# Kernel tuning notes

Hardware: AMD Instinct MI355X
Metric: run time of the kernel (lower is better)

The kernel has to match this reference:

```python
import jax, jax.numpy as jnp
import numpy as np

NUM_NEIGHBORS = 9  # cfg['num_neighbors']


def _cdist(a, b):
    """Euclidean cdist. a: [..., M, D], b: [..., N, D] -> [..., M, N]."""
    a2 = jnp.sum(a * a, axis=-1)[..., :, None]
    b2 = jnp.sum(b * b, axis=-1)[..., None, :]
    ab = jnp.einsum('...md,...nd->...mn', a, b)
    return jnp.sqrt(jnp.maximum(a2 + b2 - 2.0 * ab, 0.0))


def setup_inputs() -> dict:
    key = jax.random.key(0)
    k1, k2 = jax.random.split(key)
    B, P, D, N = 8, 784, 384, 16384
    embedding = jax.random.normal(k1, (B * P, D), dtype=jnp.float32)
    embedding_coreset = jax.random.normal(k2, (N, D), dtype=jnp.float32)
    return {"embedding": embedding, "embedding_coreset": embedding_coreset, "batch_size": B}


def reference(embedding, embedding_coreset, batch_size):
    D = embedding.shape[-1]
    # 1-NN of every patch against the coreset
    dists = _cdist(embedding, embedding_coreset)          # [B*P, N]
    patch_scores = jnp.min(dists, axis=1).reshape(batch_size, -1)   # [B, P]
    locations = jnp.argmin(dists, axis=1).reshape(batch_size, -1)   # [B, P]

    b = jnp.arange(batch_size)
    max_patches = jnp.argmax(patch_scores, axis=1)        # [B]
    emb = embedding.reshape(batch_size, -1, D)            # [B, P, D]
    max_feats = emb[b, max_patches]                       # [B, D]
    score = patch_scores[b, max_patches]                  # [B]
    nn_index = locations[b, max_patches]                  # [B]
    nn_sample = embedding_coreset[nn_index]               # [B, D]

    # k-NN of the nearest coreset sample within the coreset (support set)
    d_nn = _cdist(nn_sample, embedding_coreset)           # [B, N]
    _, support = jax.lax.top_k(-d_nn, NUM_NEIGHBORS)      # smallest dists, ascending -> [B, K]
    support_feats = embedding_coreset[support]            # [B, K, D]

    # distances from max patch feature to the support samples
    d_sup = _cdist(max_feats[:, None, :], support_feats)[:, 0, :]  # [B, K]
    weights = (1.0 - jax.nn.softmax(d_sup, axis=1))[:, 0]          # [B]
    return weights * score
```

## Files before the change

kernel.cpp:

```cpp
#include <hip/hip_runtime.h>
#include <hip/hip_bf16.h>
#include <math.h>

#define M_TOTAL 6272
#define N_CS    16384
#define D_DIM   384
#define BATCH   8
#define P_PATCH 784
#define KNN     9

#define MTILES  (M_TOTAL / 128)
#define NTILES2 (N_CS / 128)
#define NBLK    (M_TOTAL / 4)
#define PBB     196

typedef _Float16 half8 __attribute__((ext_vector_type(8)));
typedef float    floatx4 __attribute__((ext_vector_type(4)));

__device__ __forceinline__ void async_copy16(const void* g, void* l) {
    __builtin_amdgcn_global_load_lds(
        (const __attribute__((address_space(1))) void*)g,
        (__attribute__((address_space(3))) void*)l, 16, 0, 0);
}

__device__ __forceinline__ unsigned long long shfl_xor_u64(unsigned long long v, int mk) {
    int lo = __shfl_xor((int)(unsigned)v, mk, 64);
    int hi = __shfl_xor((int)(unsigned)(v >> 32), mk, 64);
    return ((unsigned long long)(unsigned)hi << 32) | (unsigned)lo;
}

__global__ void convert_all_kernel(const float* __restrict__ emb,
                                   const float* __restrict__ cs,
                                   _Float16* __restrict__ embh,
                                   _Float16* __restrict__ csh,
                                   float* __restrict__ cnorm) {
    int w = threadIdx.x >> 6, lane = threadIdx.x & 63;
    int row = blockIdx.x * 4 + w;
    if (row >= N_CS + M_TOTAL) return;
    bool is_cs = row < N_CS;
    const float* r = (is_cs ? cs + (size_t)row * D_DIM
                            : emb + (size_t)(row - N_CS) * D_DIM) + lane * 6;
    float2 a = *(const float2*)r;
    float2 b = *(const float2*)(r + 2);
    float2 c = *(const float2*)(r + 4);
    union { _Float16 h[2]; unsigned u; } p0, p1, p2;
    p0.h[0] = (_Float16)a.x; p0.h[1] = (_Float16)a.y;
    p1.h[0] = (_Float16)b.x; p1.h[1] = (_Float16)b.y;
    p2.h[0] = (_Float16)c.x; p2.h[1] = (_Float16)c.y;
    unsigned* dst = (unsigned*)(is_cs ? csh + (size_t)row * D_DIM
                                      : embh + (size_t)(row - N_CS) * D_DIM) + lane * 3;
    dst[0] = p0.u; dst[1] = p1.u; dst[2] = p2.u;
    if (is_cs) {
        float s = a.x * a.x + a.y * a.y + b.x * b.x + b.y * b.y + c.x * c.x + c.y * c.y;
#pragma unroll
        for (int mk = 1; mk <= 32; mk <<= 1) s += __shfl_xor(s, mk, 64);
        if (lane == 0) cnorm[row] = s;
    }
}

__global__ __launch_bounds__(256, 3) void mindist_mfma_kernel(
    const _Float16* __restrict__ embh, const _Float16* __restrict__ csh,
    const float* __restrict__ cnorm,
    float* __restrict__ pvals, int* __restrict__ pidx) {
    __shared__ _Float16 As[128 * 64];
    __shared__ _Float16 Bs[128 * 64];
    __shared__ float smv[128 * 2];
    __shared__ int   smi[128 * 2];

    const int b    = blockIdx.x;
    const int bx   = b >> 7;
    const int by   = ((b & 7) << 4) | ((b >> 3) & 15);
    const int tid  = threadIdx.x;
    const int lane = tid & 63;
    const int w    = tid >> 6;
    const int wr   = w >> 1, wc = w & 1;
    const int prow0 = bx * 128;
    const int nbase = by * 128;
    const int q   = lane >> 4;
    const int cl  = lane & 15;

    floatx4 acc[4][4];
#pragma unroll
    for (int mi = 0; mi < 4; ++mi)
#pragma unroll
        for (int nj = 0; nj < 4; ++nj) acc[mi][nj] = (floatx4){0.f, 0.f, 0.f, 0.f};

    const int srow = lane >> 3;
    const int scol = ((lane & 7) ^ srow) * 8;

#define STAGE(KK)                                                             \
    {                                                                         \
        _Pragma("unroll")                                                     \
        for (int i = 0; i < 8; ++i) {                                         \
            int t = (w & 1) * 8 + i;                 \
            int r = t * 8 + srow;                                             \
            if (w < 2) {                                                      \
                async_copy16(csh + (size_t)(nbase + r) * D_DIM + (KK) + scol, \
                             &As[t * 512 + lane * 8]);                        \
            } else {                                                          \
                async_copy16(embh + (size_t)(prow0 + r) * D_DIM + (KK) + scol,\
                             &Bs[t * 512 + lane * 8]);                        \
            }                                                                 \
        }                                                                     \
    }

#define COMPUTE()                                                             \
    {                                                                         \
        _Pragma("unroll")                                                     \
        for (int ks = 0; ks < 2; ++ks) {                                      \
            half8 af[4], bf[4];                                               \
            _Pragma("unroll")                                                 \
            for (int mi = 0; mi < 4; ++mi) {                                  \
                int R = wr * 64 + mi * 16 + cl;                               \
                int p = (ks * 4 + q) ^ (R & 7);                               \
                af[mi] = *(const half8*)&As[R * 64 + p * 8];                  \
            }                                                                 \
            _Pragma("unroll")                                                 \
            for (int nj = 0; nj < 4; ++nj) {                                  \
                int C = wc * 64 + nj * 16 + cl;                               \
                int p = (ks * 4 + q) ^ (C & 7);                               \
                bf[nj] = *(const half8*)&Bs[C * 64 + p * 8];                  \
            }                                                                 \
            _Pragma("unroll")                                                 \
            for (int mi = 0; mi < 4; ++mi)                                    \
                _Pragma("unroll")                                             \
                for (int nj = 0; nj < 4; ++nj)                                \
                    acc[mi][nj] = __builtin_amdgcn_mfma_f32_16x16x32_f16(     \
                        af[mi], bf[nj], acc[mi][nj], 0, 0, 0);                \
        }                                                                     \
    }

#pragma unroll 1
    for (int kk = 0; kk < D_DIM; kk += 64) {
        __syncthreads();
        STAGE(kk);
        __syncthreads();
        COMPUTE();
    }
#undef STAGE
#undef COMPUTE

    float cn16[4][4];
#pragma unroll
    for (int mi = 0; mi < 4; ++mi)
#pragma unroll
        for (int r = 0; r < 4; ++r)
            cn16[mi][r] = cnorm[nbase + wr * 64 + mi * 16 + q * 4 + r];

    const int nb_lane = nbase + wr * 64 + q * 4;
#pragma unroll
    for (int nj = 0; nj < 4; ++nj) {
        float v = 3.4e38f; int idx = 0x7fffffff;
#pragma unroll
        for (int mi = 0; mi < 4; ++mi)
#pragma unroll
            for (int r = 0; r < 4; ++r) {
                float d = cn16[mi][r] - 2.f * acc[mi][nj][r];
                if (d < v) { v = d; idx = nb_lane + mi * 16 + r; }
            }
#pragma unroll
        for (int mk = 16; mk <= 32; mk <<= 1) {
            float v2 = __shfl_xor(v, mk, 64);
            int   i2 = __shfl_xor(idx, mk, 64);
            if (v2 < v || (v2 == v && i2 < idx)) { v = v2; idx = i2; }
        }
        if (q == 0) {
            int pl = wc * 64 + nj * 16 + cl;
            smv[pl * 2 + wr] = v;
            smi[pl * 2 + wr] = idx;
        }
    }
    __syncthreads();
    if (tid < 128) {
        float v = smv[tid * 2];      int i = smi[tid * 2];
        float v1 = smv[tid * 2 + 1]; int i1 = smi[tid * 2 + 1];
        if (v1 < v) { v = v1; i = i1; }
        pvals[(size_t)(prow0 + tid) * NTILES2 + by] = v;
        pidx[(size_t)(prow0 + tid) * NTILES2 + by]  = i;
    }
}

__global__ void reduce_rescore_kernel(const float* __restrict__ pvals,
                                      const int* __restrict__ pidx,
                                      const float* __restrict__ emb,
                                      const float* __restrict__ cs,
                                      int* __restrict__ loc,
                                      unsigned long long* __restrict__ partial) {
    __shared__ unsigned long long keys[4];
    int w = threadIdx.x >> 6, lane = threadIdx.x & 63;
    int m = blockIdx.x * 4 + w;
    float v = pvals[(size_t)m * NTILES2 + lane];
    int   i = pidx[(size_t)m * NTILES2 + lane];
    {
        float v1 = pvals[(size_t)m * NTILES2 + lane + 64];
        int   i1 = pidx[(size_t)m * NTILES2 + lane + 64];
        if (v1 < v) { v = v1; i = i1; }
    }
#pragma unroll
    for (int mk = 1; mk <= 32; mk <<= 1) {
        float v2 = __shfl_xor(v, mk, 64);
        int   i2 = __shfl_xor(i, mk, 64);
        if (v2 < v || (v2 == v && i2 < i)) { v = v2; i = i2; }
    }
    const float* a = emb + (size_t)m * D_DIM;
    const float* bp = cs + (size_t)i * D_DIM;
    float s = 0.f;
#pragma unroll
    for (int t = 0; t < D_DIM / 64; ++t) {
        float d = a[lane + t * 64] - bp[lane + t * 64];
        s += d * d;
    }
#pragma unroll
    for (int mk = 1; mk <= 32; mk <<= 1) s += __shfl_xor(s, mk, 64);
    if (lane == 0) {
        float sc = sqrtf(s);
        loc[m] = i;
        int p = m % P_PATCH;
        keys[w] = ((unsigned long long)__float_as_uint(sc) << 32) |
                  (unsigned)(0x7fffffff - p);
    }
    __syncthreads();
    if (threadIdx.x == 0) {
        unsigned long long k = keys[0];
        if (keys[1] > k) k = keys[1];
        if (keys[2] > k) k = keys[2];
        if (keys[3] > k) k = keys[3];
        partial[blockIdx.x] = k;
    }
}

__global__ void dnn_kernel(const float* __restrict__ cs,
                           const float* __restrict__ cnorm,
                           const unsigned long long* __restrict__ partial,
                           const int* __restrict__ loc,
                           float* __restrict__ dmat) {
    __shared__ int bnnS[BATCH];
    {
        int bb = threadIdx.x >> 5, l32 = threadIdx.x & 31;
        unsigned long long best = 0ull;
        for (int j = l32; j < PBB; j += 32) {
            unsigned long long k = partial[bb * PBB + j];
            if (k > best) best = k;
        }
#pragma unroll
        for (int mk = 1; mk <= 16; mk <<= 1) {
            unsigned long long o = shfl_xor_u64(best, mk);
            if (o > best) best = o;
        }
        if (l32 == 0) {
            int p = 0x7fffffff - (unsigned)(best & 0xffffffffull);
            bnnS[bb] = loc[bb * P_PATCH + p];
        }
    }
    __syncthreads();

    int lane = threadIdx.x & 63;
    int gw = (blockIdx.x * 256 + threadIdx.x) >> 6;
    float qv[BATCH][6];
#pragma unroll
    for (int b = 0; b < BATCH; ++b) {
        const float* qr = cs + (size_t)bnnS[b] * D_DIM + lane * 6;
#pragma unroll
        for (int j = 0; j < 6; ++j) qv[b][j] = qr[j];
    }
    for (int n = gw; n < N_CS; n += 1024) {
        const float* r = cs + (size_t)n * D_DIM + lane * 6;
        float x[6];
#pragma unroll
        for (int j = 0; j < 6; ++j) x[j] = r[j];
        float s[BATCH];
#pragma unroll
        for (int b = 0; b < BATCH; ++b) {
            float t = 0.f;
#pragma unroll
            for (int j = 0; j < 6; ++j) t += x[j] * qv[b][j];
            s[b] = t;
        }
#pragma unroll
        for (int b = 0; b < BATCH; ++b)
#pragma unroll
            for (int mk = 1; mk <= 32; mk <<= 1) s[b] += __shfl_xor(s[b], mk, 64);
        if (lane < BATCH) {
            float sv = s[0];
#pragma unroll
            for (int b = 1; b < BATCH; ++b) sv = (lane == b) ? s[b] : sv;
            dmat[(size_t)lane * N_CS + n] = cnorm[n] - 2.f * sv;
        }
    }
}

__device__ inline void merge9(float* av, int* ai, const float* bv, const int* bi) {
    float mv[KNN]; int mi[KNN];
    int x = 0, y = 0;
#pragma unroll
    for (int k = 0; k < KNN; ++k) {
        bool ta = (av[x] < bv[y]) || (av[x] == bv[y] && ai[x] < bi[y]);
        if (ta) { mv[k] = av[x]; mi[k] = ai[x]; ++x; }
        else    { mv[k] = bv[y]; mi[k] = bi[y]; ++y; }
    }
#pragma unroll
    for (int k = 0; k < KNN; ++k) { av[k] = mv[k]; ai[k] = mi[k]; }
}

__global__ void top9_final_kernel(const float* __restrict__ dmat,
                                  const float* __restrict__ emb,
                                  const float* __restrict__ cs,
                                  const unsigned long long* __restrict__ partial,
                                  float* __restrict__ out) {
    int b = blockIdx.x;
    int tid = threadIdx.x;
    __shared__ float lv[512][KNN];
    __shared__ int   li[512][KNN];
    __shared__ float mf[D_DIM];
    __shared__ float dsup[KNN];
    __shared__ float bscoreS;
    __shared__ int   bpatchS;

    if (tid < 64) {
        unsigned long long best = 0ull;
        for (int j = tid; j < PBB; j += 64) {
            unsigned long long k = partial[b * PBB + j];
            if (k > best) best = k;
        }
#pragma unroll
        for (int mk = 1; mk <= 32; mk <<= 1) {
            unsigned long long o = shfl_xor_u64(best, mk);
            if (o > best) best = o;
        }
        if (tid == 0) {
            bpatchS = 0x7fffffff - (unsigned)(best & 0xffffffffull);
            bscoreS = __uint_as_float((unsigned)(best >> 32));
        }
    }
    __syncthreads();
    int mp = bpatchS;
    const float* frow = emb + (size_t)(b * P_PATCH + mp) * D_DIM;
    for (int i = tid; i < D_DIM; i += 512) mf[i] = frow[i];

    float tv[KNN]; int ti[KNN];
#pragma unroll
    for (int k = 0; k < KNN; ++k) { tv[k] = 3.4e38f; ti[k] = 0x7fffffff; }
    for (int n = tid; n < N_CS; n += 512) {
        float d = dmat[(size_t)b * N_CS + n];
        if (d < tv[KNN - 1] || (d == tv[KNN - 1] && n < ti[KNN - 1])) {
            tv[KNN - 1] = d; ti[KNN - 1] = n;
#pragma unroll
            for (int k = KNN - 1; k > 0; --k) {
                if (tv[k] < tv[k - 1] || (tv[k] == tv[k - 1] && ti[k] < ti[k - 1])) {
                    float fv = tv[k]; tv[k] = tv[k - 1]; tv[k - 1] = fv;
                    int   iv = ti[k]; ti[k] = ti[k - 1]; ti[k - 1] = iv;
                }
            }
        }
    }
#pragma unroll
    for (int k = 0; k < KNN; ++k) { lv[tid][k] = tv[k]; li[tid][k] = ti[k]; }
    __syncthreads();
    for (int off = 256; off > 0; off >>= 1) {
        if (tid < off) {
            float av[KNN]; int ai[KNN]; float bv2[KNN]; int bi2[KNN];
#pragma unroll
            for (int k = 0; k < KNN; ++k) {
                av[k]  = lv[tid][k];        ai[k]  = li[tid][k];
                bv2[k] = lv[tid + off][k];  bi2[k] = li[tid + off][k];
            }
            merge9(av, ai, bv2, bi2);
#pragma unroll
            for (int k = 0; k < KNN; ++k) { lv[tid][k] = av[k]; li[tid][k] = ai[k]; }
        }
        __syncthreads();
    }
    {
        int k      = tid >> 5;
        int lane32 = tid & 31;
        if (k < KNN) {
            int idx = li[0][k];
            const float* r = cs + (size_t)idx * D_DIM;
            float s = 0.f;
            for (int i = lane32; i < D_DIM; i += 32) {
                float df = mf[i] - r[i];
                s += df * df;
            }
#pragma unroll
            for (int mk = 1; mk <= 16; mk <<= 1) s += __shfl_xor(s, mk, 64);
            if (lane32 == 0) dsup[k] = sqrtf(fmaxf(s, 0.f));
        }
    }
    __syncthreads();
    if (tid == 0) {
        float mx = dsup[0];
        for (int k = 1; k < KNN; ++k) mx = fmaxf(mx, dsup[k]);
        float sum = 0.f, e0 = 0.f;
        for (int k = 0; k < KNN; ++k) {
            float e = expf(dsup[k] - mx);
            sum += e;
            if (k == 0) e0 = e;
        }
        out[b] = (1.f - e0 / sum) * bscoreS;
    }
}

extern "C" void kernel_launch(void* const* d_in, const int* in_sizes, int n_in,
                              void* d_out, int out_size, void* d_ws, size_t ws_size,
                              hipStream_t stream) {
    (void)in_sizes; (void)n_in; (void)out_size; (void)ws_size;
    const float* emb = (const float*)d_in[0];
    const float* cs  = (const float*)d_in[1];
    float* out = (float*)d_out;

    char* p = (char*)d_ws;
    float* cnorm  = (float*)p;  p += (size_t)N_CS * 4;
    float* pvals  = (float*)p;  p += (size_t)M_TOTAL * NTILES2 * 4;
    int*   pidx   = (int*)p;    p += (size_t)M_TOTAL * NTILES2 * 4;
    int*   loc    = (int*)p;    p += (size_t)M_TOTAL * 4;
    p = (char*)(((size_t)p + 7) & ~(size_t)7);
    unsigned long long* partial = (unsigned long long*)p; p += NBLK * 8;
    float* dmat   = (float*)p;  p += (size_t)BATCH * N_CS * 4;
    p = (char*)(((size_t)p + 15) & ~(size_t)15);
    _Float16* embh = (_Float16*)p; p += (size_t)M_TOTAL * D_DIM * 2;
    _Float16* csh  = (_Float16*)p; p += (size_t)N_CS * D_DIM * 2;

    {
        int rows = N_CS + M_TOTAL;
        convert_all_kernel<<<(rows + 3) / 4, 256, 0, stream>>>(emb, cs, embh, csh, cnorm);
    }
    mindist_mfma_kernel<<<MTILES * NTILES2, 256, 0, stream>>>(embh, csh, cnorm,
                                                              pvals, pidx);
    reduce_rescore_kernel<<<NBLK, 256, 0, stream>>>(pvals, pidx, emb, cs, loc, partial);
    dnn_kernel<<<256, 256, 0, stream>>>(cs, cnorm, partial, loc, dmat);
    top9_final_kernel<<<BATCH, 512, 0, stream>>>(dmat, emb, cs, partial, out);
}
```

Baseline: 252.0 us.

## Double-buffer LDS with 256x128 tiles and interleave async loads with MFMA phases

The min-distance GEMM now uses 512-thread blocks over 256 coreset by 128 patch tiles, so each block holds twice as many coreset columns and makes half as many partial results. LDS is double-buffered, and the async global-to-LDS copies for the next K tile are spread across four MFMA phases with explicit barriers, setprio and sched_barrier. This hides load latency behind compute and improves reuse of the patch tile. In exchange it uses more LDS per block and lowers occupancy, and it relies on hand-placed waitcnt and barrier ordering, which is fragile.

```diff
diff --git a/kernel.cpp b/kernel.cpp
--- a/kernel.cpp
+++ b/kernel.cpp
@@ -10,7 +10,7 @@
 #define KNN     9
 
 #define MTILES  (M_TOTAL / 128)
-#define NTILES2 (N_CS / 128)
+#define NTILES2 (N_CS / 256)
 #define NBLK    (M_TOTAL / 4)
 #define PBB     196
 
@@ -58,26 +58,30 @@
     }
 }
 
-__global__ __launch_bounds__(256, 3) void mindist_mfma_kernel(
+__global__ __launch_bounds__(512, 2) void mindist_mfma_kernel(
     const _Float16* __restrict__ embh, const _Float16* __restrict__ csh,
     const float* __restrict__ cnorm,
     float* __restrict__ pvals, int* __restrict__ pidx) {
-    __shared__ _Float16 As[128 * 64];
-    __shared__ _Float16 Bs[128 * 64];
-    __shared__ float smv[128 * 2];
-    __shared__ int   smi[128 * 2];
+    __shared__ _Float16 As0[256 * 64];
+    __shared__ _Float16 As1[256 * 64];
+    __shared__ _Float16 Bs0[128 * 64];
+    __shared__ _Float16 Bs1[128 * 64];
+    __shared__ float smv[128 * 4];
+    __shared__ int   smi[128 * 4];
 
     const int b    = blockIdx.x;
-    const int bx   = b >> 7;
-    const int by   = ((b & 7) << 4) | ((b >> 3) & 15);
+    const int bx   = b >> 6;
+    const int by   = ((b & 7) << 3) | ((b >> 3) & 7);
     const int tid  = threadIdx.x;
     const int lane = tid & 63;
     const int w    = tid >> 6;
-    const int wr   = w >> 1, wc = w & 1;
+    const int wr   = w >> 1;
+    const int wc   = w & 1;
     const int prow0 = bx * 128;
-    const int nbase = by * 128;
+    const int nbase = by * 256;
     const int q   = lane >> 4;
     const int cl  = lane & 15;
+    const int xsw = cl & 7;
 
     floatx4 acc[4][4];
 #pragma unroll
@@ -88,57 +92,84 @@
     const int srow = lane >> 3;
     const int scol = ((lane & 7) ^ srow) * 8;
 
-#define STAGE(KK)                                                             \
+#define STAGE_A(AS, KK, i)                                                    \
+    async_copy16(csh + (size_t)(nbase + (w * 4 + (i)) * 8 + srow) * D_DIM     \
+                     + (KK) + scol,                                           \
+                 &AS[(w * 4 + (i)) * 512 + lane * 8])
+#define STAGE_B(BS, KK, i)                                                    \
+    async_copy16(embh + (size_t)(prow0 + (w * 2 + (i)) * 8 + srow) * D_DIM    \
+                      + (KK) + scol,                                          \
+                 &BS[(w * 2 + (i)) * 512 + lane * 8])
+
+#define PH_BAR()                                                              \
+    do {                                                                      \
+        asm volatile("" ::: "memory");                                        \
+        __builtin_amdgcn_s_barrier();                                         \
+        asm volatile("" ::: "memory");                                        \
+    } while (0)
+#define LGKM0()  asm volatile("s_waitcnt lgkmcnt(0)" ::: "memory")
+#define WAITV0() asm volatile("s_waitcnt vmcnt(0)" ::: "memory")
+
+#define MFMA1(d, a, bb) d = __builtin_amdgcn_mfma_f32_16x16x32_f16(a, bb, d, 0, 0, 0)
+
+#define PHASE(AC, BC, ks, nh, STG, TAILW)                                     \
     {                                                                         \
-        _Pragma("unroll")                                                     \
-        for (int i = 0; i < 8; ++i) {                                         \
-            int t = (w & 1) * 8 + i;                 \
-            int r = t * 8 + srow;                                             \
-            if (w < 2) {                                                      \
-                async_copy16(csh + (size_t)(nbase + r) * D_DIM + (KK) + scol, \
-                             &As[t * 512 + lane * 8]);                        \
-            } else {                                                          \
-                async_copy16(embh + (size_t)(prow0 + r) * D_DIM + (KK) + scol,\
-                             &Bs[t * 512 + lane * 8]);                        \
-            }                                                                 \
+        if ((nh) == 0) {                                                      \
+            af0 = *(const half8*)&AC[(wr * 64 +  0 + cl) * 64 + ((((ks) * 4 + q) ^ xsw)) * 8]; \
+            af1 = *(const half8*)&AC[(wr * 64 + 16 + cl) * 64 + ((((ks) * 4 + q) ^ xsw)) * 8]; \
+            af2 = *(const half8*)&AC[(wr * 64 + 32 + cl) * 64 + ((((ks) * 4 + q) ^ xsw)) * 8]; \
+            af3 = *(const half8*)&AC[(wr * 64 + 48 + cl) * 64 + ((((ks) * 4 + q) ^ xsw)) * 8]; \
         }                                                                     \
-    }
-
-#define COMPUTE()                                                             \
+        half8 bf0 = *(const half8*)&BC[(wc * 64 + (nh) * 32 +  0 + cl) * 64 + ((((ks) * 4 + q) ^ xsw)) * 8]; \
+        half8 bf1 = *(const half8*)&BC[(wc * 64 + (nh) * 32 + 16 + cl) * 64 + ((((ks) * 4 + q) ^ xsw)) * 8]; \
+        STG;                                                                  \
+        PH_BAR();                                                             \
+        LGKM0();                                                              \
+        __builtin_amdgcn_sched_barrier(0);                                    \
+        __builtin_amdgcn_s_setprio(1);                                        \
+        MFMA1(acc[0][(nh) * 2], af0, bf0); MFMA1(acc[0][(nh) * 2 + 1], af0, bf1); \
+        MFMA1(acc[1][(nh) * 2], af1, bf0); MFMA1(acc[1][(nh) * 2 + 1], af1, bf1); \
+        MFMA1(acc[2][(nh) * 2], af2, bf0); MFMA1(acc[2][(nh) * 2 + 1], af2, bf1); \
+        MFMA1(acc[3][(nh) * 2], af3, bf0); MFMA1(acc[3][(nh) * 2 + 1], af3, bf1); \
+        __builtin_amdgcn_s_setprio(0);                                        \
+        TAILW;                                                                \
+        PH_BAR();                                                             \
+    }
+
+#define KTILE(AC, BC, S0, S1, S2, WV)                                         \
     {                                                                         \
-        _Pragma("unroll")                                                     \
-        for (int ks = 0; ks < 2; ++ks) {                                      \
-            half8 af[4], bf[4];                                               \
-            _Pragma("unroll")                                                 \
-            for (int mi = 0; mi < 4; ++mi) {                                  \
-                int R = wr * 64 + mi * 16 + cl;                               \
-                int p = (ks * 4 + q) ^ (R & 7);                               \
-                af[mi] = *(const half8*)&As[R * 64 + p * 8];                  \
-            }                                                                 \
-            _Pragma("unroll")                                                 \
-            for (int nj = 0; nj < 4; ++nj) {                                  \
-                int C = wc * 64 + nj * 16 + cl;                               \
-                int p = (ks * 4 + q) ^ (C & 7);                               \
-                bf[nj] = *(const half8*)&Bs[C * 64 + p * 8];                  \
-            }                                                                 \
-            _Pragma("unroll")                                                 \
-            for (int mi = 0; mi < 4; ++mi)                                    \
-                _Pragma("unroll")                                             \
-                for (int nj = 0; nj < 4; ++nj)                                \
-                    acc[mi][nj] = __builtin_amdgcn_mfma_f32_16x16x32_f16(     \
-                        af[mi], bf[nj], acc[mi][nj], 0, 0, 0);                \
-        }                                                                     \
-    }
+        half8 af0, af1, af2, af3;                                             \
+        PHASE(AC, BC, 0, 0, S0, {});                                          \
+        PHASE(AC, BC, 0, 1, S1, {});                                          \
+        PHASE(AC, BC, 1, 0, S2, {});                                          \
+        PHASE(AC, BC, 1, 1, {},  WV);                                         \
+    }
+
+    STAGE_A(As0, 0, 0); STAGE_A(As0, 0, 1); STAGE_A(As0, 0, 2); STAGE_A(As0, 0, 3);
+    STAGE_B(Bs0, 0, 0); STAGE_B(Bs0, 0, 1);
+    WAITV0();
+    __syncthreads();
 
 #pragma unroll 1
-    for (int kk = 0; kk < D_DIM; kk += 64) {
-        __syncthreads();
-        STAGE(kk);
-        __syncthreads();
-        COMPUTE();
-    }
-#undef STAGE
-#undef COMPUTE
+    for (int t = 0; t < 5; ++t) {
+        const int kn = (t + 1) * 64;
+        const _Float16* AC = (t & 1) ? As1 : As0;
+        const _Float16* BC = (t & 1) ? Bs1 : Bs0;
+        _Float16* AN = (t & 1) ? As0 : As1;
+        _Float16* BN = (t & 1) ? Bs0 : Bs1;
+        KTILE(AC, BC,
+              { STAGE_A(AN, kn, 0); STAGE_A(AN, kn, 1); },
+              { STAGE_A(AN, kn, 2); STAGE_A(AN, kn, 3); },
+              { STAGE_B(BN, kn, 0); STAGE_B(BN, kn, 1); },
+              WAITV0());
+    }
+    KTILE(As1, Bs1, {}, {}, {}, {});
+
+#undef KTILE
+#undef PHASE
+#undef MFMA1
+#undef STAGE_A
+#undef STAGE_B
 
     float cn16[4][4];
 #pragma unroll
@@ -166,15 +197,18 @@
         }
         if (q == 0) {
             int pl = wc * 64 + nj * 16 + cl;
-            smv[pl * 2 + wr] = v;
-            smi[pl * 2 + wr] = idx;
+            smv[pl * 4 + wr] = v;
+            smi[pl * 4 + wr] = idx;
         }
     }
     __syncthreads();
     if (tid < 128) {
-        float v = smv[tid * 2];      int i = smi[tid * 2];
-        float v1 = smv[tid * 2 + 1]; int i1 = smi[tid * 2 + 1];
-        if (v1 < v) { v = v1; i = i1; }
+        float v = smv[tid * 4]; int i = smi[tid * 4];
+#pragma unroll
+        for (int k = 1; k < 4; ++k) {
+            float v1 = smv[tid * 4 + k]; int i1 = smi[tid * 4 + k];
+            if (v1 < v) { v = v1; i = i1; }
+        }
         pvals[(size_t)(prow0 + tid) * NTILES2 + by] = v;
         pidx[(size_t)(prow0 + tid) * NTILES2 + by]  = i;
     }
@@ -191,11 +225,6 @@
     int m = blockIdx.x * 4 + w;
     float v = pvals[(size_t)m * NTILES2 + lane];
     int   i = pidx[(size_t)m * NTILES2 + lane];
-    {
-        float v1 = pvals[(size_t)m * NTILES2 + lane + 64];
-        int   i1 = pidx[(size_t)m * NTILES2 + lane + 64];
-        if (v1 < v) { v = v1; i = i1; }
-    }
 #pragma unroll
     for (int mk = 1; mk <= 32; mk <<= 1) {
         float v2 = __shfl_xor(v, mk, 64);
@@ -424,7 +453,7 @@
         int rows = N_CS + M_TOTAL;
         convert_all_kernel<<<(rows + 3) / 4, 256, 0, stream>>>(emb, cs, embh, csh, cnorm);
     }
-    mindist_mfma_kernel<<<MTILES * NTILES2, 256, 0, stream>>>(embh, csh, cnorm,
+    mindist_mfma_kernel<<<MTILES * NTILES2, 512, 0, stream>>>(embh, csh, cnorm,
                                                               pvals, pidx);
     reduce_rescore_kernel<<<NBLK, 256, 0, stream>>>(pvals, pidx, emb, cs, loc, partial);
     dnn_kernel<<<256, 256, 0, stream>>>(cs, cnorm, partial, loc, dmat);
```

New measurement: 272.2 us. 1.08x slower.

## Fuse reduce, dnn and top9 stages into one cooperative kernel with grid syncs

Applied to the files above, without the earlier changes.

Replaces three separate tail kernel launches (reduce/rescore, coreset distance, top-9 and final score) with a single cooperative kernel of 256 blocks. Grid-wide barriers separate the phases. The aim is to remove launch gaps and per-launch overhead between small tail stages. In exchange, the reduce phase now runs on only 256 blocks looping over 1568 units, the top-9 phase uses 256 threads per block instead of 512, and each grid.sync adds its own cost.

```diff
diff --git a/kernel.cpp b/kernel.cpp
--- a/kernel.cpp
+++ b/kernel.cpp
@@ -1,6 +1,9 @@
 #include <hip/hip_runtime.h>
+#include <hip/hip_cooperative_groups.h>
 #include <hip/hip_bf16.h>
 #include <math.h>
+
+namespace cg = cooperative_groups;
 
 #define M_TOTAL 6272
 #define N_CS    16384
@@ -180,63 +183,90 @@
     }
 }
 
-__global__ void reduce_rescore_kernel(const float* __restrict__ pvals,
-                                      const int* __restrict__ pidx,
-                                      const float* __restrict__ emb,
-                                      const float* __restrict__ cs,
-                                      int* __restrict__ loc,
-                                      unsigned long long* __restrict__ partial) {
-    __shared__ unsigned long long keys[4];
-    int w = threadIdx.x >> 6, lane = threadIdx.x & 63;
-    int m = blockIdx.x * 4 + w;
-    float v = pvals[(size_t)m * NTILES2 + lane];
-    int   i = pidx[(size_t)m * NTILES2 + lane];
-    {
-        float v1 = pvals[(size_t)m * NTILES2 + lane + 64];
-        int   i1 = pidx[(size_t)m * NTILES2 + lane + 64];
-        if (v1 < v) { v = v1; i = i1; }
-    }
-#pragma unroll
-    for (int mk = 1; mk <= 32; mk <<= 1) {
-        float v2 = __shfl_xor(v, mk, 64);
-        int   i2 = __shfl_xor(i, mk, 64);
-        if (v2 < v || (v2 == v && i2 < i)) { v = v2; i = i2; }
-    }
-    const float* a = emb + (size_t)m * D_DIM;
-    const float* bp = cs + (size_t)i * D_DIM;
-    float s = 0.f;
-#pragma unroll
-    for (int t = 0; t < D_DIM / 64; ++t) {
-        float d = a[lane + t * 64] - bp[lane + t * 64];
-        s += d * d;
-    }
-#pragma unroll
-    for (int mk = 1; mk <= 32; mk <<= 1) s += __shfl_xor(s, mk, 64);
-    if (lane == 0) {
-        float sc = sqrtf(s);
-        loc[m] = i;
-        int p = m % P_PATCH;
-        keys[w] = ((unsigned long long)__float_as_uint(sc) << 32) |
-                  (unsigned)(0x7fffffff - p);
-    }
-    __syncthreads();
-    if (threadIdx.x == 0) {
-        unsigned long long k = keys[0];
-        if (keys[1] > k) k = keys[1];
-        if (keys[2] > k) k = keys[2];
-        if (keys[3] > k) k = keys[3];
-        partial[blockIdx.x] = k;
-    }
-}
-
-__global__ void dnn_kernel(const float* __restrict__ cs,
-                           const float* __restrict__ cnorm,
-                           const unsigned long long* __restrict__ partial,
-                           const int* __restrict__ loc,
-                           float* __restrict__ dmat) {
+__device__ inline void merge9(float* av, int* ai, const float* bv, const int* bi) {
+    float mv[KNN]; int mi[KNN];
+    int x = 0, y = 0;
+#pragma unroll
+    for (int k = 0; k < KNN; ++k) {
+        bool ta = (av[x] < bv[y]) || (av[x] == bv[y] && ai[x] < bi[y]);
+        if (ta) { mv[k] = av[x]; mi[k] = ai[x]; ++x; }
+        else    { mv[k] = bv[y]; mi[k] = bi[y]; ++y; }
+    }
+#pragma unroll
+    for (int k = 0; k < KNN; ++k) { av[k] = mv[k]; ai[k] = mi[k]; }
+}
+
+__global__ void tail_kernel(const float* __restrict__ pvals,
+                            const int* __restrict__ pidx,
+                            const float* __restrict__ emb,
+                            const float* __restrict__ cs,
+                            const float* __restrict__ cnorm,
+                            int* __restrict__ loc,
+                            unsigned long long* __restrict__ partial,
+                            float* __restrict__ dmat,
+                            float* __restrict__ out) {
+    cg::grid_group grid = cg::this_grid();
+    const int tid = threadIdx.x;
+
+    __shared__ unsigned long long keysS[4];
     __shared__ int bnnS[BATCH];
-    {
-        int bb = threadIdx.x >> 5, l32 = threadIdx.x & 31;
+    __shared__ float lv[256][KNN];
+    __shared__ int   li[256][KNN];
+    __shared__ float mf[D_DIM];
+    __shared__ float dsup[KNN];
+    __shared__ float bscoreS;
+    __shared__ int   bpatchS;
+
+    {
+        int w = tid >> 6, lane = tid & 63;
+        for (int unit = blockIdx.x; unit < NBLK; unit += 256) {
+            int m = unit * 4 + w;
+            float v = pvals[(size_t)m * NTILES2 + lane];
+            int   i = pidx[(size_t)m * NTILES2 + lane];
+            {
+                float v1 = pvals[(size_t)m * NTILES2 + lane + 64];
+                int   i1 = pidx[(size_t)m * NTILES2 + lane + 64];
+                if (v1 < v) { v = v1; i = i1; }
+            }
+#pragma unroll
+            for (int mk = 1; mk <= 32; mk <<= 1) {
+                float v2 = __shfl_xor(v, mk, 64);
+                int   i2 = __shfl_xor(i, mk, 64);
+                if (v2 < v || (v2 == v && i2 < i)) { v = v2; i = i2; }
+            }
+            const float* a  = emb + (size_t)m * D_DIM;
+            const float* bp = cs + (size_t)i * D_DIM;
+            float s = 0.f;
+#pragma unroll
+            for (int t = 0; t < D_DIM / 64; ++t) {
+                float d = a[lane + t * 64] - bp[lane + t * 64];
+                s += d * d;
+            }
+#pragma unroll
+            for (int mk = 1; mk <= 32; mk <<= 1) s += __shfl_xor(s, mk, 64);
+            if (lane == 0) {
+                float sc = sqrtf(s);
+                loc[m] = i;
+                int p = m % P_PATCH;
+                keysS[w] = ((unsigned long long)__float_as_uint(sc) << 32) |
+                           (unsigned)(0x7fffffff - p);
+            }
+            __syncthreads();
+            if (tid == 0) {
+                unsigned long long k = keysS[0];
+                if (keysS[1] > k) k = keysS[1];
+                if (keysS[2] > k) k = keysS[2];
+                if (keysS[3] > k) k = keysS[3];
+                partial[unit] = k;
+            }
+            __syncthreads();
+        }
+    }
+    __threadfence();
+    grid.sync();
+
+    {
+        int bb = tid >> 5, l32 = tid & 31;
         unsigned long long best = 0ull;
         for (int j = l32; j < PBB; j += 32) {
             unsigned long long k = partial[bb * PBB + j];
@@ -253,68 +283,46 @@
         }
     }
     __syncthreads();
-
-    int lane = threadIdx.x & 63;
-    int gw = (blockIdx.x * 256 + threadIdx.x) >> 6;
-    float qv[BATCH][6];
-#pragma unroll
-    for (int b = 0; b < BATCH; ++b) {
-        const float* qr = cs + (size_t)bnnS[b] * D_DIM + lane * 6;
-#pragma unroll
-        for (int j = 0; j < 6; ++j) qv[b][j] = qr[j];
-    }
-    for (int n = gw; n < N_CS; n += 1024) {
-        const float* r = cs + (size_t)n * D_DIM + lane * 6;
-        float x[6];
-#pragma unroll
-        for (int j = 0; j < 6; ++j) x[j] = r[j];
-        float s[BATCH];
+    {
+        int lane = tid & 63;
+        int gw = (blockIdx.x * 256 + tid) >> 6;
+        float qv[BATCH][6];
 #pragma unroll
         for (int b = 0; b < BATCH; ++b) {
-            float t = 0.f;
-#pragma unroll
-            for (int j = 0; j < 6; ++j) t += x[j] * qv[b][j];
-            s[b] = t;
-        }
-#pragma unroll
-        for (int b = 0; b < BATCH; ++b)
-#pragma unroll
-            for (int mk = 1; mk <= 32; mk <<= 1) s[b] += __shfl_xor(s[b], mk, 64);
-        if (lane < BATCH) {
-            float sv = s[0];
-#pragma unroll
-            for (int b = 1; b < BATCH; ++b) sv = (lane == b) ? s[b] : sv;
-            dmat[(size_t)lane * N_CS + n] = cnorm[n] - 2.f * sv;
-        }
-    }
-}
-
-__device__ inline void merge9(float* av, int* ai, const float* bv, const int* bi) {
-    float mv[KNN]; int mi[KNN];
-    int x = 0, y = 0;
-#pragma unroll
-    for (int k = 0; k < KNN; ++k) {
-        bool ta = (av[x] < bv[y]) || (av[x] == bv[y] && ai[x] < bi[y]);
-        if (ta) { mv[k] = av[x]; mi[k] = ai[x]; ++x; }
-        else    { mv[k] = bv[y]; mi[k] = bi[y]; ++y; }
-    }
-#pragma unroll
-    for (int k = 0; k < KNN; ++k) { av[k] = mv[k]; ai[k] = mi[k]; }
-}
-
-__global__ void top9_final_kernel(const float* __restrict__ dmat,
-                                  const float* __restrict__ emb,
-                                  const float* __restrict__ cs,
-                                  const unsigned long long* __restrict__ partial,
-                                  float* __restrict__ out) {
-    int b = blockIdx.x;
-    int tid = threadIdx.x;
-    __shared__ float lv[512][KNN];
-    __shared__ int   li[512][KNN];
-    __shared__ float mf[D_DIM];
-    __shared__ float dsup[KNN];
-    __shared__ float bscoreS;
-    __shared__ int   bpatchS;
+            const float* qr = cs + (size_t)bnnS[b] * D_DIM + lane * 6;
+#pragma unroll
+            for (int j = 0; j < 6; ++j) qv[b][j] = qr[j];
+        }
+        for (int n = gw; n < N_CS; n += 1024) {
+            const float* r = cs + (size_t)n * D_DIM + lane * 6;
+            float x[6];
+#pragma unroll
+            for (int j = 0; j < 6; ++j) x[j] = r[j];
+            float s[BATCH];
+#pragma unroll
+            for (int b = 0; b < BATCH; ++b) {
+                float t = 0.f;
+#pragma unroll
+                for (int j = 0; j < 6; ++j) t += x[j] * qv[b][j];
+                s[b] = t;
+            }
+#pragma unroll
+            for (int b = 0; b < BATCH; ++b)
+#pragma unroll
+                for (int mk = 1; mk <= 32; mk <<= 1) s[b] += __shfl_xor(s[b], mk, 64);
+            if (lane < BATCH) {
+                float sv = s[0];
+#pragma unroll
+                for (int b = 1; b < BATCH; ++b) sv = (lane == b) ? s[b] : sv;
+                dmat[(size_t)lane * N_CS + n] = cnorm[n] - 2.f * sv;
+            }
+        }
+    }
+    __threadfence();
+    grid.sync();
+
+    if (blockIdx.x >= BATCH) return;
+    const int b = blockIdx.x;
 
     if (tid < 64) {
         unsigned long long best = 0ull;
@@ -333,14 +341,16 @@
         }
     }
     __syncthreads();
-    int mp = bpatchS;
-    const float* frow = emb + (size_t)(b * P_PATCH + mp) * D_DIM;
-    for (int i = tid; i < D_DIM; i += 512) mf[i] = frow[i];
+    {
+        int mp = bpatchS;
+        const float* frow = emb + (size_t)(b * P_PATCH + mp) * D_DIM;
+        for (int i = tid; i < D_DIM; i += 256) mf[i] = frow[i];
+    }
 
     float tv[KNN]; int ti[KNN];
 #pragma unroll
     for (int k = 0; k < KNN; ++k) { tv[k] = 3.4e38f; ti[k] = 0x7fffffff; }
-    for (int n = tid; n < N_CS; n += 512) {
+    for (int n = tid; n < N_CS; n += 256) {
         float d = dmat[(size_t)b * N_CS + n];
         if (d < tv[KNN - 1] || (d == tv[KNN - 1] && n < ti[KNN - 1])) {
             tv[KNN - 1] = d; ti[KNN - 1] = n;
@@ -356,7 +366,7 @@
 #pragma unroll
     for (int k = 0; k < KNN; ++k) { lv[tid][k] = tv[k]; li[tid][k] = ti[k]; }
     __syncthreads();
-    for (int off = 256; off > 0; off >>= 1) {
+    for (int off = 128; off > 0; off >>= 1) {
         if (tid < off) {
             float av[KNN]; int ai[KNN]; float bv2[KNN]; int bi2[KNN];
 #pragma unroll
@@ -371,19 +381,22 @@
         __syncthreads();
     }
     {
-        int k      = tid >> 5;
         int lane32 = tid & 31;
-        if (k < KNN) {
-            int idx = li[0][k];
-            const float* r = cs + (size_t)idx * D_DIM;
-            float s = 0.f;
-            for (int i = lane32; i < D_DIM; i += 32) {
-                float df = mf[i] - r[i];
-                s += df * df;
-            }
-#pragma unroll
-            for (int mk = 1; mk <= 16; mk <<= 1) s += __shfl_xor(s, mk, 64);
-            if (lane32 == 0) dsup[k] = sqrtf(fmaxf(s, 0.f));
+#pragma unroll
+        for (int kb = 0; kb < 2; ++kb) {
+            int k = (tid >> 5) + kb * 8;
+            if (k < KNN) {
+                int idx = li[0][k];
+                const float* r = cs + (size_t)idx * D_DIM;
+                float s = 0.f;
+                for (int i = lane32; i < D_DIM; i += 32) {
+                    float df = mf[i] - r[i];
+                    s += df * df;
+                }
+#pragma unroll
+                for (int mk = 1; mk <= 16; mk <<= 1) s += __shfl_xor(s, mk, 64);
+                if (lane32 == 0) dsup[k] = sqrtf(fmaxf(s, 0.f));
+            }
         }
     }
     __syncthreads();
@@ -426,7 +439,11 @@
     }
     mindist_mfma_kernel<<<MTILES * NTILES2, 256, 0, stream>>>(embh, csh, cnorm,
                                                               pvals, pidx);
-    reduce_rescore_kernel<<<NBLK, 256, 0, stream>>>(pvals, pidx, emb, cs, loc, partial);
-    dnn_kernel<<<256, 256, 0, stream>>>(cs, cnorm, partial, loc, dmat);
-    top9_final_kernel<<<BATCH, 512, 0, stream>>>(dmat, emb, cs, partial, out);
-}
+    {
+        void* args[] = {(void*)&pvals, (void*)&pidx, (void*)&emb, (void*)&cs,
+                        (void*)&cnorm, (void*)&loc, (void*)&partial,
+                        (void*)&dmat, (void*)&out};
+        hipLaunchCooperativeKernel((void*)tail_kernel, dim3(256), dim3(256),
+                                   args, 0, stream);
+    }
+}
```

After: 375.8 us. 49.1% more time.
